# Optimization experiments

Hardware: AMD Instinct MI355X
Metric: run time of the kernel (lower is better)

## Reference

```python
import jax, jax.numpy as jnp
import numpy as np

MARGIN = 1.0
N, D = 4096, 512
NUM_CLASSES = 64


def setup_inputs() -> dict:
    key = jax.random.key(0)
    k1, k2 = jax.random.split(key)
    inputs = jax.random.normal(k1, (N, D), dtype=jnp.float32)
    targets = jax.random.randint(k2, (N,), 0, NUM_CLASSES, dtype=jnp.int64)
    return {"inputs": inputs, "targets": targets}


def reference(inputs, targets):
    n = inputs.shape[0]
    sq = jnp.sum(inputs * inputs, axis=1)  # [n]
    # squared Euclidean distances, clamped at 0 (matches relu in original)
    d2 = jnp.maximum(sq[:, None] + sq[None, :] - 2.0 * (inputs @ inputs.T), 0.0)
    # safe sqrt (zero entries get 0, matching forward; avoids NaN grads)
    dist = jnp.where(d2 > 0, jnp.sqrt(jnp.where(d2 > 0, d2, 1.0)), 0.0)  # [n,n]

    same = targets[:, None] == targets[None, :]
    eye = jnp.eye(n, dtype=bool)
    pos_mask = same & ~eye          # positives, diagonal excluded
    neg_mask = ~same                # negatives (diagonal is same-label, excluded)

    # per-row sum_k exp(margin - d_ik) over negatives  (replaces per-pair loop)
    neg_sum = jnp.sum(jnp.where(neg_mask, jnp.exp(MARGIN - dist), 0.0), axis=1)  # [n]

    # J_ij = log(neg_sum_i + neg_sum_j) + d_ij for positive pairs
    J = jnp.log(neg_sum[:, None] + neg_sum[None, :]) + dist
    triu_pos = jnp.triu(pos_mask)   # loop iterated over upper-triangular positives
    hinge2 = jnp.where(triu_pos, jax.nn.relu(J) ** 2, 0.0)

    # original divides by count of ALL positive entries (both triangles)
    len_p = jnp.sum(pos_mask).astype(jnp.float32)
    return jnp.sum(hinge2) / len_p
```

## Files before the change

### kernel.cpp

```cpp
#include <hip/hip_runtime.h>
#include <math.h>

#define NN 4096
#define DD 512
#define MARGINF 1.0f
#define NCLS 64
#define MAXM 160
#define TRI (MAXM * (MAXM - 1) / 2)
#define NBLK 2080

typedef __attribute__((ext_vector_type(8))) short bf16x8;
typedef __attribute__((ext_vector_type(4))) float f32x4;

#define WS_SQ   0
#define WS_NS   4096
#define WS_LOSS 8192
#define WS_CTR  8193
#define WS_LENP 8194
#define WS_RK   8320
#define WS_MEM  12416
#define WS_XF   32768
#define WS_PD   1081344

__device__ __forceinline__ unsigned short f2bf(float f) {
    unsigned u = __float_as_uint(f);
    u += 0x7fffu + ((u >> 16) & 1u);
    return (unsigned short)(u >> 16);
}

__global__ __launch_bounds__(256) void prep_kernel(const float* __restrict__ X,
                                                   const int* __restrict__ tgt,
                                                   float* __restrict__ ws) {
    __shared__ int tg[NN];
    const int tid = threadIdx.x;
    for (int j = tid; j < NN; j += 256) tg[j] = tgt[j];

    const int wv = tid >> 6, lane = tid & 63;
    const int row = blockIdx.x * 4 + wv;
    const float4* xr = (const float4*)(X + (size_t)row * DD);
    float4 a = xr[2 * lane], b = xr[2 * lane + 1];
    float s = a.x * a.x + a.y * a.y + a.z * a.z + a.w * a.w
            + b.x * b.x + b.y * b.y + b.z * b.z + b.w * b.w;
#pragma unroll
    for (int off = 32; off; off >>= 1) s += __shfl_down(s, off, 64);

    ushort4 pa = {f2bf(a.x), f2bf(a.y), f2bf(a.z), f2bf(a.w)};
    ushort4 pb = {f2bf(b.x), f2bf(b.y), f2bf(b.z), f2bf(b.w)};
    const int r16 = row >> 4, m = row & 15;
    const int kb = lane >> 2, q = lane & 3;
    ushort4* dst = (ushort4*)((unsigned short*)(ws + WS_XF)
                              + ((size_t)(r16 * 16 + kb) * 64 + q * 16 + m) * 8);
    dst[0] = pa;
    dst[1] = pb;

    __syncthreads();
    const int myc = tg[row];
    int cnt = 0;
    for (int j = lane; j < row; j += 64) cnt += (tg[j] == myc) ? 1 : 0;
#pragma unroll
    for (int off = 32; off; off >>= 1) cnt += __shfl_down(cnt, off, 64);
    if (lane == 0) {
        ws[WS_SQ + row] = s;
        ws[WS_NS + row] = 0.0f;
        ((int*)(ws + WS_RK))[row] = cnt;
        if (cnt < MAXM) ((int*)(ws + WS_MEM))[myc * MAXM + cnt] = row;
    }
    if (blockIdx.x == 0 && tid == 0) {
        ws[WS_LOSS] = 0.0f;
        ((unsigned*)ws)[WS_CTR] = 0u;
        ws[WS_LENP] = 0.0f;
    }
}

__global__ __launch_bounds__(256, 5) void negsum_kernel(const int* __restrict__ tgt,
                                                        float* __restrict__ ws) {
    const int bidx = blockIdx.x;
    int bj = (int)((sqrtf(8.0f * (float)bidx + 1.0f) - 1.0f) * 0.5f);
    while (bj * (bj + 1) / 2 > bidx) --bj;
    while ((bj + 1) * (bj + 2) / 2 <= bidx) ++bj;
    const int bi = bidx - bj * (bj + 1) / 2;
    const int i0 = bi * 64, j0 = bj * 64;

    const int tid = threadIdx.x;
    const int w = tid >> 6, lane = tid & 63;
    const int m_ = lane & 15, q = lane >> 4;
    const int wr = (w & 1) * 32, wc = (w >> 1) * 32;
    const unsigned short* Xf = (const unsigned short*)(ws + WS_XF);

    const int air = (i0 + wr) >> 4;
    const int bjr = (j0 + wc) >> 4;
    const unsigned short* pA = Xf + (size_t)air * 8192 + lane * 8;
    const unsigned short* pB = Xf + (size_t)bjr * 8192 + lane * 8;

    f32x4 acc[2][2] = {};
    bf16x8 rgA[3][2], rgB[3][2];
#pragma unroll
    for (int s = 0; s < 2; ++s)
#pragma unroll
        for (int u = 0; u < 2; ++u) {
            rgA[s][u] = *(const bf16x8*)(pA + u * 8192 + s * 512);
            rgB[s][u] = *(const bf16x8*)(pB + u * 8192 + s * 512);
        }
#pragma unroll
    for (int it = 0; it < 16; ++it) {
        const int cur = it % 3, nx = (it + 2) % 3;
        if (it < 14) {
#pragma unroll
            for (int u = 0; u < 2; ++u) {
                rgA[nx][u] = *(const bf16x8*)(pA + u * 8192 + (it + 2) * 512);
                rgB[nx][u] = *(const bf16x8*)(pB + u * 8192 + (it + 2) * 512);
            }
        }
        acc[0][0] = __builtin_amdgcn_mfma_f32_16x16x32_bf16(rgA[cur][0], rgB[cur][0], acc[0][0], 0, 0, 0);
        acc[0][1] = __builtin_amdgcn_mfma_f32_16x16x32_bf16(rgA[cur][0], rgB[cur][1], acc[0][1], 0, 0, 0);
        acc[1][0] = __builtin_amdgcn_mfma_f32_16x16x32_bf16(rgA[cur][1], rgB[cur][0], acc[1][0], 0, 0, 0);
        acc[1][1] = __builtin_amdgcn_mfma_f32_16x16x32_bf16(rgA[cur][1], rgB[cur][1], acc[1][1], 0, 0, 0);
    }

    const float* sq = ws + WS_SQ;
    float* ns = ws + WS_NS;
    const int* rk = (const int*)(ws + WS_RK);
    float* posd = ws + WS_PD;
    float sjv[2]; int tjv[2], jv[2];
#pragma unroll
    for (int v = 0; v < 2; ++v) {
        int j = j0 + wc + v * 16 + m_;
        jv[v] = j;
        sjv[v] = sq[j];
        tjv[v] = tgt[j];
    }
    float colp[2] = {0.0f, 0.0f};
#pragma unroll
    for (int u = 0; u < 2; ++u) {
#pragma unroll
        for (int r = 0; r < 4; ++r) {
            const int i = i0 + wr + u * 16 + q * 4 + r;
            const float si = sq[i];
            const int ti = tgt[i];
            float rp = 0.0f;
#pragma unroll
            for (int v = 0; v < 2; ++v) {
                float d2 = si + sjv[v] - 2.0f * acc[u][v][r];
                float dist = d2 > 0.0f ? sqrtf(d2) : 0.0f;
                if (tjv[v] != ti) {
                    float e = __expf(MARGINF - dist);
                    rp += e;
                    colp[v] += e;
                } else if (i < jv[v]) {
                    int ra = rk[i], rb = rk[jv[v]];
                    if (ra < MAXM && rb < MAXM) {
                        int hi = ra > rb ? ra : rb;
                        int lo = ra > rb ? rb : ra;
                        posd[ti * TRI + hi * (hi - 1) / 2 + lo] = dist;
                    }
                }
            }
            rp += __shfl_xor(rp, 1, 64);
            rp += __shfl_xor(rp, 2, 64);
            rp += __shfl_xor(rp, 4, 64);
            rp += __shfl_xor(rp, 8, 64);
            if (m_ == 0) atomicAdd(&ns[i], rp);
        }
    }
    if (bi != bj) {
#pragma unroll
        for (int v = 0; v < 2; ++v) {
            float cp = colp[v];
            cp += __shfl_xor(cp, 16, 64);
            cp += __shfl_xor(cp, 32, 64);
            if (q == 0) atomicAdd(&ns[jv[v]], cp);
        }
    }
}

__global__ __launch_bounds__(256) void pair2_kernel(const int* __restrict__ tgt,
                                                    float* __restrict__ ws,
                                                    float* __restrict__ out) {
    __shared__ float wsum[4];
    __shared__ int csum[4];
    __shared__ bool last;
    const int c = blockIdx.x;
    const int tid = threadIdx.x;
    const int wv = tid >> 6, lane = tid & 63;

    int ccount = 0;
    for (int j = tid; j < NN; j += 256) ccount += (tgt[j] == c) ? 1 : 0;
#pragma unroll
    for (int off = 32; off; off >>= 1) ccount += __shfl_down(ccount, off, 64);
    if (lane == 0) csum[wv] = ccount;
    __syncthreads();
    int mc = csum[0] + csum[1] + csum[2] + csum[3];
    if (mc > MAXM) mc = MAXM;
    const int P = mc * (mc - 1) / 2;

    const int* mem = (const int*)(ws + WS_MEM) + c * MAXM;
    const float* pd = ws + WS_PD + c * TRI;
    const float* ns = ws + WS_NS;
    float lsum = 0.0f;
    for (int p = tid; p < P; p += 256) {
        int b = (int)((1.0f + sqrtf(1.0f + 8.0f * (float)p)) * 0.5f);
        while (b * (b - 1) / 2 > p) --b;
        while ((b + 1) * b / 2 <= p) ++b;
        const int a = p - b * (b - 1) / 2;
        const float dist = pd[b * (b - 1) / 2 + a];
        const int i = mem[a], j = mem[b];
        float J = __logf(ns[i] + ns[j]) + dist;
        float h = fmaxf(J, 0.0f);
        lsum += h * h;
    }
#pragma unroll
    for (int off = 32; off; off >>= 1) lsum += __shfl_xor(lsum, off, 64);
    if (lane == 0) wsum[wv] = lsum;
    __syncthreads();
    if (tid == 0) {
        float s = wsum[0] + wsum[1] + wsum[2] + wsum[3];
        if (s != 0.0f) atomicAdd(&ws[WS_LOSS], s);
        atomicAdd(&ws[WS_LENP], (float)(mc * (mc - 1)));
        __threadfence();
        unsigned d = atomicAdd((unsigned*)ws + WS_CTR, 1u);
        last = (d == NCLS - 1);
    }
    __syncthreads();
    if (last && tid == 0) {
        float total = atomicAdd(&ws[WS_LOSS], 0.0f);
        float lp = atomicAdd(&ws[WS_LENP], 0.0f);
        out[0] = total / lp;
    }
}

extern "C" void kernel_launch(void* const* d_in, const int* in_sizes, int n_in,
                              void* d_out, int out_size, void* d_ws, size_t ws_size,
                              hipStream_t stream) {
    const float* X  = (const float*)d_in[0];
    const int*  tgt = (const int*)d_in[1];
    float* ws  = (float*)d_ws;
    float* out = (float*)d_out;

    hipLaunchKernelGGL(prep_kernel, dim3(NN / 4), dim3(256), 0, stream, X, tgt, ws);
    hipLaunchKernelGGL(negsum_kernel, dim3(NBLK), dim3(256), 0, stream, tgt, ws);
    hipLaunchKernelGGL(pair2_kernel, dim3(NCLS), dim3(256), 0, stream, tgt, ws, out);
}
```

Baseline: 116.8 us.

## Replace negsum atomics with per-tile partial sums reduced in pair kernel

Each negsum tile now writes its row and column partial exp-sums to a dedicated slot in a [N x 128] partials buffer instead of using atomicAdd on a shared per-row accumulator. The pair kernel reduces each class member's 128 partials into shared memory before the hinge loop, which also removes the zero-initialisation in prep. The GEMM prefetch pipeline drops from triple to double buffering and the occupancy hint rises from 5 to 6 to lower register pressure. This trades atomic contention for an extra 2 MB of partial-sum traffic and a less deeply pipelined load stage.

```diff
diff --git a/kernel.cpp b/kernel.cpp
--- a/kernel.cpp
+++ b/kernel.cpp
@@ -13,14 +13,14 @@
 typedef __attribute__((ext_vector_type(4))) float f32x4;
 
 #define WS_SQ   0
-#define WS_NS   4096
 #define WS_LOSS 8192
 #define WS_CTR  8193
 #define WS_LENP 8194
 #define WS_RK   8320
 #define WS_MEM  12416
-#define WS_XF   32768
-#define WS_PD   1081344
+#define WS_P    32768
+#define WS_XF   557056
+#define WS_PD   1605632
 
 __device__ __forceinline__ unsigned short f2bf(float f) {
     unsigned u = __float_as_uint(f);
@@ -61,7 +61,6 @@
     for (int off = 32; off; off >>= 1) cnt += __shfl_down(cnt, off, 64);
     if (lane == 0) {
         ws[WS_SQ + row] = s;
-        ws[WS_NS + row] = 0.0f;
         ((int*)(ws + WS_RK))[row] = cnt;
         if (cnt < MAXM) ((int*)(ws + WS_MEM))[myc * MAXM + cnt] = row;
     }
@@ -72,7 +71,7 @@
     }
 }
 
-__global__ __launch_bounds__(256, 5) void negsum_kernel(const int* __restrict__ tgt,
+__global__ __launch_bounds__(256, 6) void negsum_kernel(const int* __restrict__ tgt,
                                                         float* __restrict__ ws) {
     const int bidx = blockIdx.x;
     int bj = (int)((sqrtf(8.0f * (float)bidx + 1.0f) - 1.0f) * 0.5f);
@@ -93,34 +92,35 @@
     const unsigned short* pB = Xf + (size_t)bjr * 8192 + lane * 8;
 
     f32x4 acc[2][2] = {};
-    bf16x8 rgA[3][2], rgB[3][2];
-#pragma unroll
-    for (int s = 0; s < 2; ++s)
-#pragma unroll
-        for (int u = 0; u < 2; ++u) {
-            rgA[s][u] = *(const bf16x8*)(pA + u * 8192 + s * 512);
-            rgB[s][u] = *(const bf16x8*)(pB + u * 8192 + s * 512);
-        }
+    bf16x8 af[2], bfr[2], nA[2], nB[2];
+#pragma unroll
+    for (int u = 0; u < 2; ++u) {
+        af[u]  = *(const bf16x8*)(pA + u * 8192);
+        bfr[u] = *(const bf16x8*)(pB + u * 8192);
+    }
 #pragma unroll
     for (int it = 0; it < 16; ++it) {
-        const int cur = it % 3, nx = (it + 2) % 3;
-        if (it < 14) {
+        if (it < 15) {
 #pragma unroll
             for (int u = 0; u < 2; ++u) {
-                rgA[nx][u] = *(const bf16x8*)(pA + u * 8192 + (it + 2) * 512);
-                rgB[nx][u] = *(const bf16x8*)(pB + u * 8192 + (it + 2) * 512);
+                nA[u] = *(const bf16x8*)(pA + u * 8192 + (it + 1) * 512);
+                nB[u] = *(const bf16x8*)(pB + u * 8192 + (it + 1) * 512);
             }
         }
-        acc[0][0] = __builtin_amdgcn_mfma_f32_16x16x32_bf16(rgA[cur][0], rgB[cur][0], acc[0][0], 0, 0, 0);
-        acc[0][1] = __builtin_amdgcn_mfma_f32_16x16x32_bf16(rgA[cur][0], rgB[cur][1], acc[0][1], 0, 0, 0);
-        acc[1][0] = __builtin_amdgcn_mfma_f32_16x16x32_bf16(rgA[cur][1], rgB[cur][0], acc[1][0], 0, 0, 0);
-        acc[1][1] = __builtin_amdgcn_mfma_f32_16x16x32_bf16(rgA[cur][1], rgB[cur][1], acc[1][1], 0, 0, 0);
+        acc[0][0] = __builtin_amdgcn_mfma_f32_16x16x32_bf16(af[0], bfr[0], acc[0][0], 0, 0, 0);
+        acc[0][1] = __builtin_amdgcn_mfma_f32_16x16x32_bf16(af[0], bfr[1], acc[0][1], 0, 0, 0);
+        acc[1][0] = __builtin_amdgcn_mfma_f32_16x16x32_bf16(af[1], bfr[0], acc[1][0], 0, 0, 0);
+        acc[1][1] = __builtin_amdgcn_mfma_f32_16x16x32_bf16(af[1], bfr[1], acc[1][1], 0, 0, 0);
+#pragma unroll
+        for (int u = 0; u < 2; ++u) { af[u] = nA[u]; bfr[u] = nB[u]; }
     }
 
     const float* sq = ws + WS_SQ;
-    float* ns = ws + WS_NS;
+    float* P = ws + WS_P;
     const int* rk = (const int*)(ws + WS_RK);
     float* posd = ws + WS_PD;
+    const int hrow = wc >> 5;
+    const int hcol = wr >> 5;
     float sjv[2]; int tjv[2], jv[2];
 #pragma unroll
     for (int v = 0; v < 2; ++v) {
@@ -159,7 +159,7 @@
             rp += __shfl_xor(rp, 2, 64);
             rp += __shfl_xor(rp, 4, 64);
             rp += __shfl_xor(rp, 8, 64);
-            if (m_ == 0) atomicAdd(&ns[i], rp);
+            if (m_ == 0) P[(size_t)i * 128 + bj * 2 + hrow] = rp;
         }
     }
     if (bi != bj) {
@@ -168,7 +168,7 @@
             float cp = colp[v];
             cp += __shfl_xor(cp, 16, 64);
             cp += __shfl_xor(cp, 32, 64);
-            if (q == 0) atomicAdd(&ns[jv[v]], cp);
+            if (q == 0) P[(size_t)jv[v] * 128 + bi * 2 + hcol] = cp;
         }
     }
 }
@@ -176,6 +176,7 @@
 __global__ __launch_bounds__(256) void pair2_kernel(const int* __restrict__ tgt,
                                                     float* __restrict__ ws,
                                                     float* __restrict__ out) {
+    __shared__ float nsm[MAXM];
     __shared__ float wsum[4];
     __shared__ int csum[4];
     __shared__ bool last;
@@ -191,20 +192,28 @@
     __syncthreads();
     int mc = csum[0] + csum[1] + csum[2] + csum[3];
     if (mc > MAXM) mc = MAXM;
-    const int P = mc * (mc - 1) / 2;
-
+    const int P_ = mc * (mc - 1) / 2;
     const int* mem = (const int*)(ws + WS_MEM) + c * MAXM;
+    const float* Pp = ws + WS_P;
+
+    for (int p = wv; p < mc; p += 4) {
+        const float* row = Pp + (size_t)mem[p] * 128;
+        float v = row[lane] + row[lane + 64];
+#pragma unroll
+        for (int off = 32; off; off >>= 1) v += __shfl_xor(v, off, 64);
+        if (lane == 0) nsm[p] = v;
+    }
+    __syncthreads();
+
     const float* pd = ws + WS_PD + c * TRI;
-    const float* ns = ws + WS_NS;
     float lsum = 0.0f;
-    for (int p = tid; p < P; p += 256) {
+    for (int p = tid; p < P_; p += 256) {
         int b = (int)((1.0f + sqrtf(1.0f + 8.0f * (float)p)) * 0.5f);
         while (b * (b - 1) / 2 > p) --b;
         while ((b + 1) * b / 2 <= p) ++b;
         const int a = p - b * (b - 1) / 2;
         const float dist = pd[b * (b - 1) / 2 + a];
-        const int i = mem[a], j = mem[b];
-        float J = __logf(ns[i] + ns[j]) + dist;
+        float J = __logf(nsm[a] + nsm[b]) + dist;
         float h = fmaxf(J, 0.0f);
         lsum += h * h;
     }
```

Measured after the change: 124.3 us. +6.4%, slower.
